# Kernel optimization log

Hardware: AMD Instinct MI355X
Metric: run time of the kernel (lower is better)

## Reference

```python
import jax, jax.numpy as jnp
import numpy as np

T, H = 4096, 2048

def _glorot(key, shape):
    return jax.random.uniform(key, shape, minval=-1.0, maxval=1.0) * jnp.sqrt(2.0 / sum(shape))

def setup_inputs() -> dict:
    key = jax.random.key(0)
    k_x, k_a, k_b = jax.random.split(key, 3)
    x_seq = jax.random.normal(k_x, (T, H), dtype=jnp.float32)
    a_diag = _glorot(k_a, (H,)).astype(jnp.float32)        # (H,)
    b_mat = _glorot(k_b, (H, H)).astype(jnp.float32)       # (H, H)
    return {"x_seq": x_seq, "a_diag": a_diag, "b_mat": b_mat}

def _power_kernel(a_diag, length):
    # kernel[h, k] = a_diag[h] ** k for k in [0, length).
    # Computed via cumprod (identical math to jnp.power with integer exponents,
    # but well-defined for negative a_diag and differentiable).
    h = a_diag.shape[0]
    ones = jnp.ones((h, 1), dtype=a_diag.dtype)
    pows = jnp.cumprod(jnp.broadcast_to(a_diag[:, None], (h, length - 1)), axis=1)
    return jnp.concatenate([ones, pows], axis=1)[:, None, :]  # (H, 1, T)

def reference(x_seq, a_diag, b_mat):
    seq_len, hidden_size = x_seq.shape
    s = b_mat.T @ x_seq.T                                  # (H, T)
    s_padded = jnp.pad(s, ((0, 0), (seq_len - 1, 0)))[None, :, :]  # (1, H, 2T-1)
    kernel = _power_kernel(a_diag, seq_len)                # (H, 1, T)
    kernel_flipped = jnp.flip(kernel, axis=-1)
    conv_out = jax.lax.conv_general_dilated(
        s_padded, kernel_flipped,
        window_strides=(1,), padding="VALID",
        dimension_numbers=("NCT", "OIT", "NCT"),
        feature_group_count=hidden_size,
    )                                                      # (1, H, T)
    return conv_out[0].T                                   # (T, H)
```

## Files before the change

kernel.cpp:

```cpp
#include <hip/hip_runtime.h>
#include <cstdint>
#include <cstddef>

typedef short bf16x8 __attribute__((ext_vector_type(8)));
typedef float f32x4 __attribute__((ext_vector_type(4)));

__device__ __forceinline__ unsigned short f2bf(float f) {
    union { float f; uint32_t u; } v; v.f = f;
    uint32_t r = v.u + 0x7FFFu + ((v.u >> 16) & 1u);
    return (unsigned short)(r >> 16);
}

__device__ __forceinline__ float bf2f(unsigned short u) {
    union { uint32_t u; float f; } v; v.u = (uint32_t)u << 16;
    return v.f;
}


__global__ void prep_kernel(const float* __restrict__ X,
                            unsigned short* __restrict__ Xbf, int n4,
                            const float* __restrict__ B,
                            unsigned short* __restrict__ Bt, int H,
                            int castBlocks) {
    if ((int)blockIdx.x < castBlocks) {
        int i = blockIdx.x * 256 + threadIdx.x;
        if (i < n4) {
            float4 v = ((const float4*)X)[i];
            ushort4 o;
            o.x = f2bf(v.x); o.y = f2bf(v.y); o.z = f2bf(v.z); o.w = f2bf(v.w);
            ((ushort4*)Xbf)[i] = o;
        }
        return;
    }
    __shared__ float tile[32][33];
    int tb = blockIdx.x - castBlocks;
    int tilesPerRow = H / 32;
    int bx = (tb % tilesPerRow) * 32;
    int by = (tb / tilesPerRow) * 32;
    int tx = threadIdx.x & 31, ty = threadIdx.x >> 5;
#pragma unroll
    for (int i = 0; i < 32; i += 8)
        tile[ty + i][tx] = B[(size_t)(by + ty + i) * H + bx + tx];
    __syncthreads();
#pragma unroll
    for (int i = 0; i < 32; i += 8)
        Bt[(size_t)(bx + ty + i) * H + by + tx] = f2bf(tile[tx][ty + i]);
}


__device__ __forceinline__ void stage_tile(
    const unsigned short* __restrict__ Ab, const unsigned short* __restrict__ Bb,
    unsigned short* sAp, unsigned short* sBp,
    int wave, int srow, int scol, int k0, int K)
{
#pragma unroll
    for (int i = 0; i < 4; ++i) {
        const int t = wave * 4 + i;
        const unsigned short* ga = Ab + (size_t)(t * 8 + srow) * K + (k0 + scol);
        __builtin_amdgcn_global_load_lds(
            (const __attribute__((address_space(1))) void*)ga,
            (__attribute__((address_space(3))) void*)(sAp + t * 512),
            16, 0, 0);
        const unsigned short* gb = Bb + (size_t)(t * 8 + srow) * K + (k0 + scol);
        __builtin_amdgcn_global_load_lds(
            (const __attribute__((address_space(1))) void*)gb,
            (__attribute__((address_space(3))) void*)(sBp + t * 512),
            16, 0, 0);
    }
}


__global__ __launch_bounds__(256, 4) void gemm_sk_bf16out(
    const unsigned short* __restrict__ A,
    const unsigned short* __restrict__ Bt,
    unsigned short* __restrict__ S0, unsigned short* __restrict__ S1,
    int M, int N, int K, int gridM, int gridN)
{
    __shared__ __attribute__((aligned(16))) unsigned short sA[128 * 64];
    __shared__ __attribute__((aligned(16))) unsigned short sB[128 * 64];

    const int tid  = threadIdx.x;
    const int wave = tid >> 6;
    const int lane = tid & 63;

    int b = blockIdx.x;
    int mt, nt, kt;
    if ((gridM & 7) == 0) {
        int x = b & 7, g = b >> 3;
        int mPerX = gridM >> 3;
        int ml = g % mPerX, g2 = g / mPerX;
        nt = g2 % gridN;
        kt = g2 / gridN;
        mt = x * mPerX + ml;
    } else {
        mt = b % gridM;
        nt = (b / gridM) % gridN;
        kt = b / (gridM * gridN);
    }
    const int m0 = mt * 128;
    const int n0 = nt * 128;
    const int ksize = K / 2;
    const int kbase = kt * ksize;

    const int srow = lane >> 3;
    const int scol = ((lane & 7) ^ srow) * 8;

    const int quad = lane >> 4;
    const int l16  = lane & 15;
    const int wm = wave >> 1;
    const int wn = wave & 1;

    const int s7 = l16 & 7;
    const int rbaseA = (wm * 8 + (l16 >> 3)) * 1024 + s7 * 128;
    const int rbaseB = (wn * 8 + (l16 >> 3)) * 1024 + s7 * 128;
    const int coff0 = (quad ^ s7) * 16;
    const int coff1 = ((quad + 4) ^ s7) * 16;

    f32x4 acc[4][4];
#pragma unroll
    for (int i = 0; i < 4; ++i)
#pragma unroll
        for (int j = 0; j < 4; ++j)
            acc[i][j] = (f32x4){0.f, 0.f, 0.f, 0.f};

    const unsigned short* Ab = A  + (size_t)m0 * K;
    const unsigned short* Bb = Bt + (size_t)n0 * K;

    for (int k0 = kbase; k0 < kbase + ksize; k0 += 64) {
        stage_tile(Ab, Bb, sA, sB, wave, srow, scol, k0, K);
        __syncthreads();
        bf16x8 af[2][4], bfr[2][4];
#pragma unroll
        for (int t = 0; t < 4; ++t) {
            const char* pa = (const char*)sA + rbaseA + t * 2048;
            af[0][t]  = *(const bf16x8*)(pa + coff0);
            af[1][t]  = *(const bf16x8*)(pa + coff1);
            const char* pb = (const char*)sB + rbaseB + t * 2048;
            bfr[0][t] = *(const bf16x8*)(pb + coff0);
            bfr[1][t] = *(const bf16x8*)(pb + coff1);
        }
#pragma unroll
        for (int kk = 0; kk < 2; ++kk)
#pragma unroll
            for (int im = 0; im < 4; ++im)
#pragma unroll
                for (int in = 0; in < 4; ++in)
                    acc[im][in] = __builtin_amdgcn_mfma_f32_16x16x32_bf16(
                        af[kk][im], bfr[kk][in], acc[im][in], 0, 0, 0);
        __syncthreads();
    }

    unsigned short* __restrict__ S = (kt == 0) ? S0 : S1;
#pragma unroll
    for (int im = 0; im < 4; ++im) {
#pragma unroll
        for (int in = 0; in < 4; ++in) {
            int col = n0 + wn * 64 + in * 16 + l16;
#pragma unroll
            for (int r = 0; r < 4; ++r) {
                int row = m0 + wm * 64 + im * 16 + quad * 4 + r;
                S[(size_t)row * N + col] = f2bf(acc[im][in][r]);
            }
        }
    }
}

__global__ __launch_bounds__(256, 4) void gemm_f32out(
    const unsigned short* __restrict__ A,
    const unsigned short* __restrict__ Bt,
    float* __restrict__ C, int M, int N, int K, int gridM)
{
    __shared__ __attribute__((aligned(16))) unsigned short sA[128 * 64];
    __shared__ __attribute__((aligned(16))) unsigned short sB[128 * 64];

    const int tid  = threadIdx.x;
    const int wave = tid >> 6;
    const int lane = tid & 63;

    int b = blockIdx.x;
    int mt, nt;
    if ((gridM & 7) == 0) {
        int x = b & 7, g = b >> 3;
        int mPerX = gridM >> 3;
        mt = x * mPerX + (g % mPerX);
        nt = g / mPerX;
    } else {
        mt = b % gridM;
        nt = b / gridM;
    }
    const int m0 = mt * 128;
    const int n0 = nt * 128;

    const int srow = lane >> 3;
    const int scol = ((lane & 7) ^ srow) * 8;
    const int quad = lane >> 4;
    const int l16  = lane & 15;
    const int wm = wave >> 1;
    const int wn = wave & 1;
    const int s7 = l16 & 7;
    const int rbaseA = (wm * 8 + (l16 >> 3)) * 1024 + s7 * 128;
    const int rbaseB = (wn * 8 + (l16 >> 3)) * 1024 + s7 * 128;
    const int coff0 = (quad ^ s7) * 16;
    const int coff1 = ((quad + 4) ^ s7) * 16;

    f32x4 acc[4][4];
#pragma unroll
    for (int i = 0; i < 4; ++i)
#pragma unroll
        for (int j = 0; j < 4; ++j)
            acc[i][j] = (f32x4){0.f, 0.f, 0.f, 0.f};

    const unsigned short* Ab = A  + (size_t)m0 * K;
    const unsigned short* Bb = Bt + (size_t)n0 * K;

    for (int k0 = 0; k0 < K; k0 += 64) {
        stage_tile(Ab, Bb, sA, sB, wave, srow, scol, k0, K);
        __syncthreads();
        bf16x8 af[2][4], bfr[2][4];
#pragma unroll
        for (int t = 0; t < 4; ++t) {
            const char* pa = (const char*)sA + rbaseA + t * 2048;
            af[0][t]  = *(const bf16x8*)(pa + coff0);
            af[1][t]  = *(const bf16x8*)(pa + coff1);
            const char* pb = (const char*)sB + rbaseB + t * 2048;
            bfr[0][t] = *(const bf16x8*)(pb + coff0);
            bfr[1][t] = *(const bf16x8*)(pb + coff1);
        }
#pragma unroll
        for (int kk = 0; kk < 2; ++kk)
#pragma unroll
            for (int im = 0; im < 4; ++im)
#pragma unroll
                for (int in = 0; in < 4; ++in)
                    acc[im][in] = __builtin_amdgcn_mfma_f32_16x16x32_bf16(
                        af[kk][im], bfr[kk][in], acc[im][in], 0, 0, 0);
        __syncthreads();
    }

#pragma unroll
    for (int im = 0; im < 4; ++im)
#pragma unroll
        for (int in = 0; in < 4; ++in) {
            int col = n0 + wn * 64 + in * 16 + l16;
#pragma unroll
            for (int r = 0; r < 4; ++r) {
                int row = m0 + wm * 64 + im * 16 + quad * 4 + r;
                C[(size_t)row * N + col] = acc[im][in][r];
            }
        }
}


__global__ void scan_splitk_bf16(const unsigned short* __restrict__ S0,
                                 const unsigned short* __restrict__ S1,
                                 const float* __restrict__ a_diag,
                                 float* __restrict__ out,
                                 int H2, int chunk) {
    int tid = blockIdx.x * blockDim.x + threadIdx.x;
    int hp = tid % H2, c = tid / H2;
    float2 av = ((const float2*)a_diag)[hp];
    const ushort2* S0v = (const ushort2*)S0;
    const ushort2* S1v = (const ushort2*)S1;
    float2* outv = (float2*)out;

    float y0 = 0.f, y1 = 0.f;
    if (c > 0) {
        size_t r0 = (size_t)c * chunk - 8;
#pragma unroll
        for (int i = 0; i < 8; ++i) {
            size_t idx = (r0 + i) * H2 + hp;
            ushort2 u = S0v[idx], w = S1v[idx];
            y0 = fmaf(av.x, y0, bf2f(u.x) + bf2f(w.x));
            y1 = fmaf(av.y, y1, bf2f(u.y) + bf2f(w.y));
        }
    }
    size_t idx = (size_t)c * chunk * H2 + hp;
    ushort2 u = S0v[idx], w = S1v[idx];
    for (int t = 0; t < chunk - 1; ++t) {
        size_t idx2 = idx + H2;
        ushort2 un = S0v[idx2], wn = S1v[idx2];
        y0 = fmaf(av.x, y0, bf2f(u.x) + bf2f(w.x));
        y1 = fmaf(av.y, y1, bf2f(u.y) + bf2f(w.y));
        outv[idx] = make_float2(y0, y1);
        u = un; w = wn; idx = idx2;
    }
    y0 = fmaf(av.x, y0, bf2f(u.x) + bf2f(w.x));
    y1 = fmaf(av.y, y1, bf2f(u.y) + bf2f(w.y));
    outv[idx] = make_float2(y0, y1);
}


__global__ void scan_init_kernel(const float* __restrict__ S,
                                 const float* __restrict__ a_diag,
                                 float* __restrict__ yinit,
                                 int H, int chunk, int W) {
    int tid = blockIdx.x * blockDim.x + threadIdx.x;
    int h = tid % H, c = tid / H;
    float a = a_diag[h];
    float y = 0.f;
    if (c > 0) {
        int t0 = c * chunk;
        for (int t = t0 - W; t < t0; ++t)
            y = fmaf(a, y, S[(size_t)t * H + h]);
    }
    yinit[(size_t)c * H + h] = y;
}

__global__ void scan_run_kernel(const float* __restrict__ yinit,
                                const float* __restrict__ a_diag,
                                float* __restrict__ out,
                                int H, int chunk) {
    int tid = blockIdx.x * blockDim.x + threadIdx.x;
    int h = tid % H, c = tid / H;
    float a = a_diag[h];
    float y = yinit[(size_t)c * H + h];
    size_t base = (size_t)c * chunk * H + h;
    float s = out[base];
#pragma unroll 4
    for (int t = 0; t < chunk - 1; ++t) {
        float snext = out[base + (size_t)(t + 1) * H];
        y = fmaf(a, y, s);
        out[base + (size_t)t * H] = y;
        s = snext;
    }
    y = fmaf(a, y, s);
    out[base + (size_t)(chunk - 1) * H] = y;
}


__global__ void gemm_fallback(const float* __restrict__ X, const float* __restrict__ B,
                              float* __restrict__ C, int M, int N, int K) {
    __shared__ float sA[16][17];
    __shared__ float sB[16][17];
    int tx = threadIdx.x, ty = threadIdx.y;
    int row = blockIdx.y * 16 + ty, col = blockIdx.x * 16 + tx;
    float acc = 0.f;
    for (int k0 = 0; k0 < K; k0 += 16) {
        sA[ty][tx] = (row < M && k0 + tx < K) ? X[(size_t)row * K + k0 + tx] : 0.f;
        sB[ty][tx] = (k0 + ty < K && col < N) ? B[(size_t)(k0 + ty) * N + col] : 0.f;
        __syncthreads();
#pragma unroll
        for (int kk = 0; kk < 16; ++kk) acc += sA[ty][kk] * sB[kk][tx];
        __syncthreads();
    }
    if (row < M && col < N) C[(size_t)row * N + col] = acc;
}

__global__ void scan_serial(float* __restrict__ out, const float* __restrict__ a_diag,
                            int T, int H) {
    int h = blockIdx.x * blockDim.x + threadIdx.x;
    if (h >= H) return;
    float a = a_diag[h], y = 0.f;
    for (int t = 0; t < T; ++t) {
        y = fmaf(a, y, out[(size_t)t * H + h]);
        out[(size_t)t * H + h] = y;
    }
}


extern "C" void kernel_launch(void* const* d_in, const int* in_sizes, int n_in,
                              void* d_out, int out_size, void* d_ws, size_t ws_size,
                              hipStream_t stream) {
    const float* x = (const float*)d_in[0];
    const float* a = (const float*)d_in[1];
    const float* b = (const float*)d_in[2];
    float* out = (float*)d_out;

    const int H = in_sizes[1];
    const int T = in_sizes[0] / H;
    const int M = T, N = H, K = H;

    const int CHUNK = 32, W = 12;

    size_t xbf_elems = (size_t)M * K;
    size_t bt_elems  = (size_t)N * K;
    size_t MN = (size_t)M * N;
    int nchunks = (T % CHUNK == 0) ? T / CHUNK : 0;

    size_t need_sk  = (xbf_elems + bt_elems + 2 * MN) * 2 + 256;
    size_t need_mid = xbf_elems * 2 + bt_elems * 2 + 256;

    bool shape_ok = (M % 128 == 0) && (N % 128 == 0) && (K % 128 == 0) &&
                    (H % 32 == 0) && nchunks > 0 && ((xbf_elems % 4) == 0) &&
                    (((size_t)nchunks * H) % 256 == 0);
    int gridM = M / 128, gridN = N / 128;

    int n4 = (int)(xbf_elems / 4);
    int castBlocks = (n4 + 255) / 256;
    int transBlocks = (H % 32 == 0) ? (H / 32) * (H / 32) : 0;

    int H2 = H / 2;
    size_t nth2 = (size_t)nchunks * H2;

    if (shape_ok && (gridM % 8 == 0) && (H % 4 == 0) &&
        (nth2 % 256 == 0) && ws_size >= need_sk) {
        unsigned short* Xbf = (unsigned short*)d_ws;
        unsigned short* Bt  = Xbf + xbf_elems;
        unsigned short* S0  = Bt + bt_elems;
        unsigned short* S1  = S0 + MN;

        prep_kernel<<<castBlocks + transBlocks, 256, 0, stream>>>(
            x, Xbf, n4, b, Bt, H, castBlocks);

        gemm_sk_bf16out<<<gridM * gridN * 2, 256, 0, stream>>>(
            Xbf, Bt, S0, S1, M, N, K, gridM, gridN);

        scan_splitk_bf16<<<(int)(nth2 / 256), 256, 0, stream>>>(
            S0, S1, a, out, H2, CHUNK);
    } else if (shape_ok && ws_size >= need_mid &&
               ((size_t)nchunks * H * 4 <= xbf_elems * 2)) {
        unsigned short* Xbf = (unsigned short*)d_ws;
        unsigned short* Bt  = Xbf + xbf_elems;
        float* yinit = (float*)d_ws;

        prep_kernel<<<castBlocks + transBlocks, 256, 0, stream>>>(
            x, Xbf, n4, b, Bt, H, castBlocks);

        gemm_f32out<<<gridM * gridN, 256, 0, stream>>>(
            Xbf, Bt, out, M, N, K, gridM);

        int nth = nchunks * H;
        scan_init_kernel<<<nth / 256, 256, 0, stream>>>(out, a, yinit, H, CHUNK, W);
        scan_run_kernel<<<nth / 256, 256, 0, stream>>>(yinit, a, out, H, CHUNK);
    } else {
        dim3 tb(16, 16), tg((N + 15) / 16, (M + 15) / 16);
        gemm_fallback<<<tg, tb, 0, stream>>>(x, b, out, M, N, K);
        scan_serial<<<(H + 255) / 256, 256, 0, stream>>>(out, a, T, H);
    }
}
```

Baseline: 143.2 us.

## Enlarge split-K GEMM tile to 256x128 and halve scan chunk size

The split-K bf16 GEMM now computes 256x128 output tiles. Each wave holds 8x4 accumulator fragments and uses a per-kk fragment load loop, which raises arithmetic intensity per LDS stage and halves the number of blocks. Launch bounds drop to 2 blocks per CU to allow the higher register use. The scan CHUNK also changes from 32 to 16, which doubles scan parallelism. The cost is lower occupancy, fewer blocks to spread across CUs, and a larger register footprint.

```diff
diff --git a/kernel.cpp b/kernel.cpp
--- a/kernel.cpp
+++ b/kernel.cpp
@@ -48,35 +48,13 @@
 }
 
 
-__device__ __forceinline__ void stage_tile(
-    const unsigned short* __restrict__ Ab, const unsigned short* __restrict__ Bb,
-    unsigned short* sAp, unsigned short* sBp,
-    int wave, int srow, int scol, int k0, int K)
-{
-#pragma unroll
-    for (int i = 0; i < 4; ++i) {
-        const int t = wave * 4 + i;
-        const unsigned short* ga = Ab + (size_t)(t * 8 + srow) * K + (k0 + scol);
-        __builtin_amdgcn_global_load_lds(
-            (const __attribute__((address_space(1))) void*)ga,
-            (__attribute__((address_space(3))) void*)(sAp + t * 512),
-            16, 0, 0);
-        const unsigned short* gb = Bb + (size_t)(t * 8 + srow) * K + (k0 + scol);
-        __builtin_amdgcn_global_load_lds(
-            (const __attribute__((address_space(1))) void*)gb,
-            (__attribute__((address_space(3))) void*)(sBp + t * 512),
-            16, 0, 0);
-    }
-}
-
-
-__global__ __launch_bounds__(256, 4) void gemm_sk_bf16out(
+__global__ __launch_bounds__(256, 2) void gemm_sk_bf16out(
     const unsigned short* __restrict__ A,
     const unsigned short* __restrict__ Bt,
     unsigned short* __restrict__ S0, unsigned short* __restrict__ S1,
     int M, int N, int K, int gridM, int gridN)
 {
-    __shared__ __attribute__((aligned(16))) unsigned short sA[128 * 64];
+    __shared__ __attribute__((aligned(16))) unsigned short sA[256 * 64];
     __shared__ __attribute__((aligned(16))) unsigned short sB[128 * 64];
 
     const int tid  = threadIdx.x;
@@ -97,7 +75,7 @@
         nt = (b / gridM) % gridN;
         kt = b / (gridM * gridN);
     }
-    const int m0 = mt * 128;
+    const int m0 = mt * 256;
     const int n0 = nt * 128;
     const int ksize = K / 2;
     const int kbase = kt * ksize;
@@ -109,16 +87,13 @@
     const int l16  = lane & 15;
     const int wm = wave >> 1;
     const int wn = wave & 1;
-
     const int s7 = l16 & 7;
-    const int rbaseA = (wm * 8 + (l16 >> 3)) * 1024 + s7 * 128;
-    const int rbaseB = (wn * 8 + (l16 >> 3)) * 1024 + s7 * 128;
-    const int coff0 = (quad ^ s7) * 16;
-    const int coff1 = ((quad + 4) ^ s7) * 16;
-
-    f32x4 acc[4][4];
-#pragma unroll
-    for (int i = 0; i < 4; ++i)
+    const int c0 = (quad ^ s7) * 16;
+    const int c1 = ((quad + 4) ^ s7) * 16;
+
+    f32x4 acc[8][4];
+#pragma unroll
+    for (int i = 0; i < 8; ++i)
 #pragma unroll
         for (int j = 0; j < 4; ++j)
             acc[i][j] = (f32x4){0.f, 0.f, 0.f, 0.f};
@@ -126,42 +101,84 @@
     const unsigned short* Ab = A  + (size_t)m0 * K;
     const unsigned short* Bb = Bt + (size_t)n0 * K;
 
+    const int rA = (wm * 16 + (l16 >> 3)) * 1024 + s7 * 128;
+    const int rB = (wn * 8  + (l16 >> 3)) * 1024 + s7 * 128;
+
     for (int k0 = kbase; k0 < kbase + ksize; k0 += 64) {
-        stage_tile(Ab, Bb, sA, sB, wave, srow, scol, k0, K);
-        __syncthreads();
-        bf16x8 af[2][4], bfr[2][4];
-#pragma unroll
-        for (int t = 0; t < 4; ++t) {
-            const char* pa = (const char*)sA + rbaseA + t * 2048;
-            af[0][t]  = *(const bf16x8*)(pa + coff0);
-            af[1][t]  = *(const bf16x8*)(pa + coff1);
-            const char* pb = (const char*)sB + rbaseB + t * 2048;
-            bfr[0][t] = *(const bf16x8*)(pb + coff0);
-            bfr[1][t] = *(const bf16x8*)(pb + coff1);
-        }
-#pragma unroll
-        for (int kk = 0; kk < 2; ++kk)
-#pragma unroll
-            for (int im = 0; im < 4; ++im)
+#pragma unroll
+        for (int i = 0; i < 8; ++i) {
+            const int t = wave * 8 + i;
+            const unsigned short* ga = Ab + (size_t)(t * 8 + srow) * K + (k0 + scol);
+            __builtin_amdgcn_global_load_lds(
+                (const __attribute__((address_space(1))) void*)ga,
+                (__attribute__((address_space(3))) void*)(sA + t * 512),
+                16, 0, 0);
+        }
+#pragma unroll
+        for (int i = 0; i < 4; ++i) {
+            const int t = wave * 4 + i;
+            const unsigned short* gb = Bb + (size_t)(t * 8 + srow) * K + (k0 + scol);
+            __builtin_amdgcn_global_load_lds(
+                (const __attribute__((address_space(1))) void*)gb,
+                (__attribute__((address_space(3))) void*)(sB + t * 512),
+                16, 0, 0);
+        }
+        __syncthreads();
+
+#pragma unroll
+        for (int kk = 0; kk < 2; ++kk) {
+            const int co = kk ? c1 : c0;
+            bf16x8 af[8], bfr[4];
+#pragma unroll
+            for (int im = 0; im < 8; ++im)
+                af[im] = *(const bf16x8*)((const char*)sA + rA + im * 2048 + co);
+#pragma unroll
+            for (int in = 0; in < 4; ++in)
+                bfr[in] = *(const bf16x8*)((const char*)sB + rB + in * 2048 + co);
+#pragma unroll
+            for (int im = 0; im < 8; ++im)
 #pragma unroll
                 for (int in = 0; in < 4; ++in)
                     acc[im][in] = __builtin_amdgcn_mfma_f32_16x16x32_bf16(
-                        af[kk][im], bfr[kk][in], acc[im][in], 0, 0, 0);
+                        af[im], bfr[in], acc[im][in], 0, 0, 0);
+        }
         __syncthreads();
     }
 
     unsigned short* __restrict__ S = (kt == 0) ? S0 : S1;
 #pragma unroll
-    for (int im = 0; im < 4; ++im) {
+    for (int im = 0; im < 8; ++im) {
 #pragma unroll
         for (int in = 0; in < 4; ++in) {
             int col = n0 + wn * 64 + in * 16 + l16;
 #pragma unroll
             for (int r = 0; r < 4; ++r) {
-                int row = m0 + wm * 64 + im * 16 + quad * 4 + r;
+                int row = m0 + wm * 128 + im * 16 + quad * 4 + r;
                 S[(size_t)row * N + col] = f2bf(acc[im][in][r]);
             }
         }
+    }
+}
+
+
+__device__ __forceinline__ void stage_tile128(
+    const unsigned short* __restrict__ Ab, const unsigned short* __restrict__ Bb,
+    unsigned short* sAp, unsigned short* sBp,
+    int wave, int srow, int scol, int k0, int K)
+{
+#pragma unroll
+    for (int i = 0; i < 4; ++i) {
+        const int t = wave * 4 + i;
+        const unsigned short* ga = Ab + (size_t)(t * 8 + srow) * K + (k0 + scol);
+        __builtin_amdgcn_global_load_lds(
+            (const __attribute__((address_space(1))) void*)ga,
+            (__attribute__((address_space(3))) void*)(sAp + t * 512),
+            16, 0, 0);
+        const unsigned short* gb = Bb + (size_t)(t * 8 + srow) * K + (k0 + scol);
+        __builtin_amdgcn_global_load_lds(
+            (const __attribute__((address_space(1))) void*)gb,
+            (__attribute__((address_space(3))) void*)(sBp + t * 512),
+            16, 0, 0);
     }
 }
 
@@ -214,7 +231,7 @@
     const unsigned short* Bb = Bt + (size_t)n0 * K;
 
     for (int k0 = 0; k0 < K; k0 += 64) {
-        stage_tile(Ab, Bb, sA, sB, wave, srow, scol, k0, K);
+        stage_tile128(Ab, Bb, sA, sB, wave, srow, scol, k0, K);
         __syncthreads();
         bf16x8 af[2][4], bfr[2][4];
 #pragma unroll
@@ -370,7 +387,7 @@
     const int T = in_sizes[0] / H;
     const int M = T, N = H, K = H;
 
-    const int CHUNK = 32, W = 12;
+    const int CHUNK = 16, W = 12;
 
     size_t xbf_elems = (size_t)M * K;
     size_t bt_elems  = (size_t)N * K;
@@ -383,7 +400,9 @@
     bool shape_ok = (M % 128 == 0) && (N % 128 == 0) && (K % 128 == 0) &&
                     (H % 32 == 0) && nchunks > 0 && ((xbf_elems % 4) == 0) &&
                     (((size_t)nchunks * H) % 256 == 0);
-    int gridM = M / 128, gridN = N / 128;
+    int gridMf = M / 128;
+    int gridM  = (M % 256 == 0) ? M / 256 : 0;
+    int gridN  = N / 128;
 
     int n4 = (int)(xbf_elems / 4);
     int castBlocks = (n4 + 255) / 256;
@@ -392,7 +411,7 @@
     int H2 = H / 2;
     size_t nth2 = (size_t)nchunks * H2;
 
-    if (shape_ok && (gridM % 8 == 0) && (H % 4 == 0) &&
+    if (shape_ok && gridM > 0 && (gridM % 8 == 0) && (H % 4 == 0) &&
         (nth2 % 256 == 0) && ws_size >= need_sk) {
         unsigned short* Xbf = (unsigned short*)d_ws;
         unsigned short* Bt  = Xbf + xbf_elems;
@@ -416,8 +435,8 @@
         prep_kernel<<<castBlocks + transBlocks, 256, 0, stream>>>(
             x, Xbf, n4, b, Bt, H, castBlocks);
 
-        gemm_f32out<<<gridM * gridN, 256, 0, stream>>>(
-            Xbf, Bt, out, M, N, K, gridM);
+        gemm_f32out<<<gridMf * gridN, 256, 0, stream>>>(
+            Xbf, Bt, out, M, N, K, gridMf);
 
         int nth = nchunks * H;
         scan_init_kernel<<<nth / 256, 256, 0, stream>>>(out, a, yinit, H, CHUNK, W);
```

New measurement: 140.4 us. About the same (-1.9%).
